# Performance work log

Hardware: AMD Instinct MI355X
Metric: run time of the kernel (lower is better)

The kernel has to match this reference:

```python
import jax, jax.numpy as jnp
import numpy as np

N = 4096
DIM_IN = 256
DIM_H = DIM_IN // 2  # 128
DIM_OUT = 128


def setup_inputs() -> dict:
    key = jax.random.key(0)
    ks = jax.random.split(key, 8)
    # Normalized-adjacency-like dense matrices (scaled so propagation is stable
    # and exp() of the score matrix does not overflow).
    A_s = jax.random.uniform(ks[0], (N, N), dtype=jnp.float32) * (1.0 / N)
    A_t = jax.random.uniform(ks[1], (N, N), dtype=jnp.float32) * (1.0 / N)
    X_s = jax.random.normal(ks[2], (N, DIM_IN), dtype=jnp.float32) * 0.1
    X_t = jax.random.normal(ks[3], (N, DIM_IN), dtype=jnp.float32) * 0.1
    # Linear weights (bias=False). Stored as [in, out] for x @ W.
    W1 = jax.random.normal(ks[4], (DIM_IN, DIM_H), dtype=jnp.float32) / np.sqrt(DIM_IN)
    W2 = jax.random.normal(ks[5], (DIM_H, DIM_H), dtype=jnp.float32) / np.sqrt(DIM_H)
    W3 = jax.random.normal(ks[6], (DIM_H, DIM_H), dtype=jnp.float32) / np.sqrt(DIM_H)
    W4 = jax.random.normal(ks[7], (DIM_H, DIM_OUT), dtype=jnp.float32) / np.sqrt(DIM_H)
    return {"A_s": A_s, "X_s": X_s, "A_t": A_t, "X_t": X_t,
            "W1": W1, "W2": W2, "W3": W3, "W4": W4}


def reference(A_s, X_s, A_t, X_t, W1, W2, W3, W4):
    # Two GCN propagation layers per graph: relu((A @ X) @ W)
    Xs = jax.nn.relu((A_s @ X_s) @ W1)   # [N, DIM_H]
    Xs = jax.nn.relu((A_s @ Xs) @ W2)    # [N, DIM_H]
    Xt = jax.nn.relu((A_t @ X_t) @ W1)
    Xt = jax.nn.relu((A_t @ Xt) @ W2)
    # Unnormalized exp cross-attention scores: [N, N]
    S = jnp.exp((Xs @ W3) @ Xt.T)
    out_s = (S @ Xs) @ W4                # [N, DIM_OUT]
    out_t = (S @ Xt) @ W4                # [N, DIM_OUT]
    return (out_s, out_t, S)
```

## Files before the change

kernel.cpp:

```cpp
#include <hip/hip_runtime.h>
#include <stdint.h>

typedef __attribute__((ext_vector_type(4))) float f32x4;
typedef __attribute__((ext_vector_type(8))) short s16x8;

typedef const __attribute__((address_space(1))) void* gas_ptr;
typedef __attribute__((address_space(3))) void* las_ptr;

__device__ __forceinline__ unsigned short f2b(float f) {
    union { float f; unsigned u; } v; v.f = f;
    unsigned r = v.u + 0x7fffu + ((v.u >> 16) & 1u);
    return (unsigned short)(r >> 16);
}

__device__ __forceinline__ unsigned pack2(float f0, float f1) {
    union { float f; unsigned u; } a, b;
    a.f = f0; b.f = f1;
    return __builtin_amdgcn_perm(b.u + 0x8000u, a.u + 0x8000u, 0x07060302u);
}

__global__ void cast2_bf16_k(const float* __restrict__ a, unsigned short* __restrict__ da,
                             const float* __restrict__ b, unsigned short* __restrict__ db,
                             int n4) {
    int i = blockIdx.x * blockDim.x + threadIdx.x;
    int stride = gridDim.x * blockDim.x;
    for (; i < n4; i += stride) {
        float4 va = ((const float4*)a)[i];
        ushort4 pa; pa.x = f2b(va.x); pa.y = f2b(va.y); pa.z = f2b(va.z); pa.w = f2b(va.w);
        ((ushort4*)da)[i] = pa;
        float4 vb = ((const float4*)b)[i];
        ushort4 pb; pb.x = f2b(vb.x); pb.y = f2b(vb.y); pb.z = f2b(vb.z); pb.w = f2b(vb.w);
        ((ushort4*)db)[i] = pb;
    }
}

__global__ void reduce8_relu_cast_k(const float* __restrict__ P, unsigned short* __restrict__ d,
                                    int n4, int slice4) {
    int i = blockIdx.x * blockDim.x + threadIdx.x;
    int stride = gridDim.x * blockDim.x;
    for (; i < n4; i += stride) {
        f32x4 s = ((const f32x4*)P)[i];
        #pragma unroll
        for (int z = 1; z < 8; z++) s += ((const f32x4*)P)[i + (size_t)z * slice4];
        ushort4 p;
        p.x = f2b(fmaxf(s[0], 0.f)); p.y = f2b(fmaxf(s[1], 0.f));
        p.z = f2b(fmaxf(s[2], 0.f)); p.w = f2b(fmaxf(s[3], 0.f));
        ((ushort4*)d)[i] = p;
    }
}

__global__ void reduce8_fold_k(const float* __restrict__ P, float* __restrict__ out) {
    const int n4 = 4096 * 256 / 4;
    int i = blockIdx.x * blockDim.x + threadIdx.x;
    int stride = gridDim.x * blockDim.x;
    for (; i < n4; i += stride) {
        f32x4 s = ((const f32x4*)P)[i];
        #pragma unroll
        for (int z = 1; z < 8; z++) s += ((const f32x4*)P)[i + (size_t)z * n4];
        const int m = i >> 6;
        const int c = (i & 63) << 2;
        float* o = out + ((c >> 7) ? (size_t)4096 * 128 : 0) + (size_t)m * 128 + (c & 127);
        *(f32x4*)(void*)o = s;
    }
}

__global__ void transpose_w_k(const float* __restrict__ W1, const float* __restrict__ W2,
                              const float* __restrict__ W3, const float* __restrict__ W4,
                              unsigned short* __restrict__ W1t, unsigned short* __restrict__ W2t,
                              unsigned short* __restrict__ W3t, unsigned short* __restrict__ W4t) {
    __shared__ float tile[32][33];
    const float* src; unsigned short* dst; int R, C;
    switch (blockIdx.z) {
        case 0: src = W1; dst = W1t; R = 256; C = 128; break;
        case 1: src = W2; dst = W2t; R = 128; C = 128; break;
        case 2: src = W3; dst = W3t; R = 128; C = 128; break;
        default: src = W4; dst = W4t; R = 128; C = 128; break;
    }
    int c0 = blockIdx.x * 32, r0 = blockIdx.y * 32;
    if (r0 >= R) return;
    int tx = threadIdx.x & 31, ty = threadIdx.x >> 5;
    #pragma unroll
    for (int rr = ty; rr < 32; rr += 8)
        tile[rr][tx] = src[(size_t)(r0 + rr) * C + c0 + tx];
    __syncthreads();
    #pragma unroll
    for (int rr = ty; rr < 32; rr += 8)
        dst[(size_t)(c0 + rr) * R + r0 + tx] = f2b(tile[tx][rr]);
}

enum { EP_BF16 = 0, EP_T = 1, EP_TFOLD = 2, EP_EXP = 3, EP_PART = 4 };

template<int BM, int BN, int FM, int FN, int EPI>
__global__ void __launch_bounds__(256)
gemm_nt(const unsigned short* __restrict__ A, const unsigned short* __restrict__ B,
        int lda, int ldb, int kchunk,
        float* __restrict__ Cf, unsigned short* __restrict__ Cb,
        unsigned short* __restrict__ Ct, int ldc, int ldct)
{
    __shared__ __align__(16) short As[BM * 32];
    __shared__ __align__(16) short Bs[BN * 32];

    const int t = threadIdx.x;
    const int lane = t & 63;
    const int w = t >> 6;
    const int wr = w >> 1, wc = w & 1;
    const int m0 = blockIdx.x * BM;
    const int n0 = blockIdx.y * BN;
    const int k0 = blockIdx.z * kchunk;

    f32x4 acc[FM][FN];
    #pragma unroll
    for (int i = 0; i < FM; i++)
        #pragma unroll
        for (int j = 0; j < FN; j++) acc[i][j] = (f32x4){0.f, 0.f, 0.f, 0.f};

    const int KT = kchunk >> 5;
    const int mrow = lane & 15;
    const int q8 = (lane >> 4) << 3;

    for (int kt = 0; kt < KT; ++kt) {
        const int kk = k0 + (kt << 5);
        #pragma unroll
        for (int idx = t; idx < BM * 4; idx += 256) {
            const unsigned short* g = A + (size_t)(m0 + (idx >> 2)) * lda + kk + ((idx & 3) << 3);
            __builtin_amdgcn_global_load_lds((gas_ptr)g, (las_ptr)(As + idx * 8), 16, 0, 0);
        }
        #pragma unroll
        for (int idx = t; idx < BN * 4; idx += 256) {
            const unsigned short* g = B + (size_t)(n0 + (idx >> 2)) * ldb + kk + ((idx & 3) << 3);
            __builtin_amdgcn_global_load_lds((gas_ptr)g, (las_ptr)(Bs + idx * 8), 16, 0, 0);
        }
        __syncthreads();

        s16x8 af[FM], bfr[FN];
        #pragma unroll
        for (int i = 0; i < FM; i++)
            af[i] = *(const s16x8*)(const void*)(As + (wr * FM * 16 + i * 16 + mrow) * 32 + q8);
        #pragma unroll
        for (int j = 0; j < FN; j++)
            bfr[j] = *(const s16x8*)(const void*)(Bs + (wc * FN * 16 + j * 16 + mrow) * 32 + q8);
        #pragma unroll
        for (int i = 0; i < FM; i++)
            #pragma unroll
            for (int j = 0; j < FN; j++)
                acc[i][j] = __builtin_amdgcn_mfma_f32_16x16x32_bf16(af[i], bfr[j], acc[i][j], 0, 0, 0);
        __syncthreads();
    }

    const int cn = lane & 15;
    const int q4 = (lane >> 4) << 2;
    #pragma unroll
    for (int i = 0; i < FM; i++) {
        const int mb = m0 + wr * FM * 16 + i * 16 + q4;
        #pragma unroll
        for (int j = 0; j < FN; j++) {
            const int nn = n0 + wc * FN * 16 + j * 16 + cn;
            if constexpr (EPI == EP_BF16) {
                #pragma unroll
                for (int r = 0; r < 4; r++)
                    Cb[(size_t)(mb + r) * ldc + nn] = f2b(acc[i][j][r]);
            } else if constexpr (EPI == EP_T) {
                ushort4 p;
                p.x = f2b(acc[i][j][0]); p.y = f2b(acc[i][j][1]);
                p.z = f2b(acc[i][j][2]); p.w = f2b(acc[i][j][3]);
                *(ushort4*)(void*)(Ct + (size_t)nn * ldct + mb) = p;
            } else if constexpr (EPI == EP_TFOLD) {
                ushort4 p;
                p.x = f2b(acc[i][j][0]); p.y = f2b(acc[i][j][1]);
                p.z = f2b(acc[i][j][2]); p.w = f2b(acc[i][j][3]);
                const int trow = nn + ((mb >> 12) << 7);
                *(ushort4*)(void*)(Ct + (size_t)trow * ldct + (mb & 4095)) = p;
            } else if constexpr (EPI == EP_EXP) {
                #pragma unroll
                for (int r = 0; r < 4; r++) {
                    float v = __expf(acc[i][j][r]);
                    Cf[(size_t)(mb + r) * ldc + nn] = v;
                    Cb[(size_t)(mb + r) * ldc + nn] = f2b(v);
                }
            } else if constexpr (EPI == EP_PART) {
                float* base = Cf + (size_t)blockIdx.z * ((size_t)4096 * 256);
                #pragma unroll
                for (int r = 0; r < 4; r++)
                    base[(size_t)(mb + r) * ldc + nn] = acc[i][j][r];
            }
        }
    }
}

__global__ void __launch_bounds__(256)
pz_fused(const unsigned short* __restrict__ X2,
         const unsigned short* __restrict__ W3t, const unsigned short* __restrict__ W4t,
         unsigned short* __restrict__ Pb, unsigned short* __restrict__ ZcatT)
{
    const bool isP = (blockIdx.y == 1);
    if (isP && blockIdx.x >= 128) return;
    const unsigned short* B = isP ? W3t : W4t;

    __shared__ __align__(16) short As[32 * 32];
    __shared__ __align__(16) short Bs[128 * 32];

    const int t = threadIdx.x;
    const int lane = t & 63;
    const int w = t >> 6;
    const int wr = w >> 1, wc = w & 1;
    const int m0 = blockIdx.x * 32;

    f32x4 acc[4];
    #pragma unroll
    for (int j = 0; j < 4; j++) acc[j] = (f32x4){0.f, 0.f, 0.f, 0.f};

    const int mrow = lane & 15;
    const int q8 = (lane >> 4) << 3;

    for (int kt = 0; kt < 4; ++kt) {
        const int kk = kt << 5;
        if (t < 128) {
            const unsigned short* g = X2 + (size_t)(m0 + (t >> 2)) * 128 + kk + ((t & 3) << 3);
            __builtin_amdgcn_global_load_lds((gas_ptr)g, (las_ptr)(As + t * 8), 16, 0, 0);
        }
        #pragma unroll
        for (int idx = t; idx < 512; idx += 256) {
            const unsigned short* g = B + (size_t)(idx >> 2) * 128 + kk + ((idx & 3) << 3);
            __builtin_amdgcn_global_load_lds((gas_ptr)g, (las_ptr)(Bs + idx * 8), 16, 0, 0);
        }
        __syncthreads();

        s16x8 af = *(const s16x8*)(const void*)(As + (wr * 16 + mrow) * 32 + q8);
        #pragma unroll
        for (int j = 0; j < 4; j++) {
            s16x8 bf = *(const s16x8*)(const void*)(Bs + (wc * 64 + j * 16 + mrow) * 32 + q8);
            acc[j] = __builtin_amdgcn_mfma_f32_16x16x32_bf16(af, bf, acc[j], 0, 0, 0);
        }
        __syncthreads();
    }

    const int cn = lane & 15;
    const int q4 = (lane >> 4) << 2;
    const int mb = m0 + wr * 16 + q4;
    #pragma unroll
    for (int j = 0; j < 4; j++) {
        const int nn = wc * 64 + j * 16 + cn;
        if (isP) {
            #pragma unroll
            for (int r = 0; r < 4; r++)
                Pb[(size_t)(mb + r) * 128 + nn] = f2b(acc[j][r]);
        } else {
            ushort4 p;
            p.x = f2b(acc[j][0]); p.y = f2b(acc[j][1]);
            p.z = f2b(acc[j][2]); p.w = f2b(acc[j][3]);
            const int trow = nn + ((mb >> 12) << 7);
            *(ushort4*)(void*)(ZcatT + (size_t)trow * 4096 + (mb & 4095)) = p;
        }
    }
}

__global__ void __launch_bounds__(256)
gemm_a32_nt(const float* __restrict__ A, const float* __restrict__ A2,
            const unsigned short* __restrict__ B, const unsigned short* __restrict__ B2,
            int Mhalf, int lda, int ldb, int kchunk, float* __restrict__ Cf, int ldc)
{
    __shared__ __align__(16) float As[64 * 32];
    __shared__ __align__(16) short Bs[128 * 32];

    const int t = threadIdx.x;
    const int lane = t & 63;
    const int w = t >> 6;
    const int wr = w >> 1, wc = w & 1;
    const int m0 = blockIdx.x * 64;
    const int n0 = blockIdx.y * 128;
    const int k0 = blockIdx.z * kchunk;

    const float* Ap = A;
    const unsigned short* Bp = B;
    int am0 = m0;
    if (m0 >= Mhalf) { Ap = A2; Bp = B2; am0 = m0 - Mhalf; }

    f32x4 acc[2][4];
    #pragma unroll
    for (int i = 0; i < 2; i++)
        #pragma unroll
        for (int j = 0; j < 4; j++) acc[i][j] = (f32x4){0.f, 0.f, 0.f, 0.f};

    const int KT = kchunk >> 5;
    const int mrow = lane & 15;
    const int q8 = (lane >> 4) << 3;
    const int q2 = (lane >> 4) << 1;

    for (int kt = 0; kt < KT; ++kt) {
        const int kk = k0 + (kt << 5);
        #pragma unroll
        for (int it = 0; it < 2; ++it) {
            int idx = it * 256 + t;
            int row = idx >> 3, grp = idx & 7;
            const float* g = Ap + (size_t)(am0 + row) * lda + kk + ((grp ^ (row & 7)) << 2);
            __builtin_amdgcn_global_load_lds((gas_ptr)g, (las_ptr)(As + idx * 4), 16, 0, 0);
        }
        #pragma unroll
        for (int it = 0; it < 2; ++it) {
            int idx = it * 256 + t;
            const unsigned short* g = Bp + (size_t)(n0 + (idx >> 2)) * ldb + kk + ((idx & 3) << 3);
            __builtin_amdgcn_global_load_lds((gas_ptr)g, (las_ptr)(Bs + idx * 8), 16, 0, 0);
        }
        __syncthreads();

        s16x8 af[2], bfr[4];
        #pragma unroll
        for (int i = 0; i < 2; i++) {
            const int r = wr * 32 + i * 16 + mrow;
            const f32x4 lo = *(const f32x4*)(const void*)(As + r * 32 + ((q2 ^ (r & 7)) << 2));
            const f32x4 hi = *(const f32x4*)(const void*)(As + r * 32 + (((q2 | 1) ^ (r & 7)) << 2));
            union { s16x8 v; unsigned u[4]; } pk;
            pk.u[0] = pack2(lo[0], lo[1]); pk.u[1] = pack2(lo[2], lo[3]);
            pk.u[2] = pack2(hi[0], hi[1]); pk.u[3] = pack2(hi[2], hi[3]);
            af[i] = pk.v;
        }
        #pragma unroll
        for (int j = 0; j < 4; j++)
            bfr[j] = *(const s16x8*)(const void*)(Bs + (wc * 64 + j * 16 + mrow) * 32 + q8);
        #pragma unroll
        for (int i = 0; i < 2; i++)
            #pragma unroll
            for (int j = 0; j < 4; j++)
                acc[i][j] = __builtin_amdgcn_mfma_f32_16x16x32_bf16(af[i], bfr[j], acc[i][j], 0, 0, 0);
        __syncthreads();
    }

    float* base = Cf + (size_t)blockIdx.z * ((size_t)8192 * 128);
    const int cn = lane & 15;
    const int q4 = (lane >> 4) << 2;
    #pragma unroll
    for (int i = 0; i < 2; i++) {
        const int mb = m0 + wr * 32 + i * 16 + q4;
        #pragma unroll
        for (int j = 0; j < 4; j++) {
            const int nn = n0 + wc * 64 + j * 16 + cn;
            #pragma unroll
            for (int r = 0; r < 4; r++)
                base[(size_t)(mb + r) * ldc + nn] = acc[i][j][r];
        }
    }
}

extern "C" void kernel_launch(void* const* d_in, const int* in_sizes, int n_in,
                              void* d_out, int out_size, void* d_ws, size_t ws_size,
                              hipStream_t stream) {
    const int N = 4096;
    const float* A_s = (const float*)d_in[0];
    const float* X_s = (const float*)d_in[1];
    const float* A_t = (const float*)d_in[2];
    const float* X_t = (const float*)d_in[3];
    const float* W1  = (const float*)d_in[4];
    const float* W2  = (const float*)d_in[5];
    const float* W3  = (const float*)d_in[6];
    const float* W4  = (const float*)d_in[7];

    float* out   = (float*)d_out;
    float* S_out = out + (size_t)2 * N * 128;

    char* ws = (char*)d_ws;
    unsigned short* Xcatb = (unsigned short*)(ws + 0);
    unsigned short* W1t   = (unsigned short*)(ws + 4194304);
    unsigned short* W2t   = (unsigned short*)(ws + 4259840);
    unsigned short* W3t   = (unsigned short*)(ws + 4292608);
    unsigned short* W4t   = (unsigned short*)(ws + 4325376);
    unsigned short* Y1T   = (unsigned short*)(ws + 4718592);
    unsigned short* X1b   = (unsigned short*)(ws + 6815744);
    unsigned short* X2b   = (unsigned short*)(ws + 8912896);
    unsigned short* Pb    = (unsigned short*)(ws + 11010048);
    unsigned short* ZcatT = (unsigned short*)(ws + 12058624);
    float*          Pf    = (float*)(ws + 14155776);
    unsigned short* Sb    = (unsigned short*)(ws + 47710208);
    unsigned short* Xt2b  = X2b + (size_t)N * 128;

    cast2_bf16_k<<<512, 256, 0, stream>>>(X_s, Xcatb, X_t, Xcatb + (size_t)N * 256, N * 256 / 4);
    transpose_w_k<<<dim3(4, 8, 4), 256, 0, stream>>>(W1, W2, W3, W4, W1t, W2t, W3t, W4t);

    gemm_nt<32, 128, 1, 4, EP_T><<<dim3(256, 1, 1), 256, 0, stream>>>(
        Xcatb, W1t, 256, 256, 256, nullptr, nullptr, Y1T, 0, 8192);

    gemm_a32_nt<<<dim3(128, 1, 8), 256, 0, stream>>>(
        A_s, A_t, Y1T, Y1T + 4096, 4096, 4096, 8192, 512, Pf, 128);
    reduce8_relu_cast_k<<<1024, 256, 0, stream>>>(Pf, X1b, 8192 * 128 / 4, 8192 * 128 / 4);

    gemm_nt<32, 128, 1, 4, EP_T><<<dim3(256, 1, 1), 256, 0, stream>>>(
        X1b, W2t, 128, 128, 128, nullptr, nullptr, Y1T, 0, 8192);

    gemm_a32_nt<<<dim3(128, 1, 8), 256, 0, stream>>>(
        A_s, A_t, Y1T, Y1T + 4096, 4096, 4096, 8192, 512, Pf, 128);
    reduce8_relu_cast_k<<<1024, 256, 0, stream>>>(Pf, X2b, 8192 * 128 / 4, 8192 * 128 / 4);

    pz_fused<<<dim3(256, 2, 1), 256, 0, stream>>>(X2b, W3t, W4t, Pb, ZcatT);

    gemm_nt<128, 128, 4, 4, EP_EXP><<<dim3(32, 32, 1), 256, 0, stream>>>(
        Pb, Xt2b, 128, 128, 128, S_out, Sb, nullptr, 4096, 0);

    gemm_nt<64, 128, 2, 4, EP_PART><<<dim3(64, 2, 8), 256, 0, stream>>>(
        Sb, ZcatT, 4096, 4096, 512, Pf, nullptr, nullptr, 256, 0);
    reduce8_fold_k<<<1024, 256, 0, stream>>>(Pf, out);
}
```

Before: 312.2 us.

## Unify GEMMs into register-loaded A with wide swizzled LDS B stages

Replaces the separate bf16 and fp32-A GEMM kernels with one templated kernel. A fragments are read straight from global memory into registers, with fp32-to-bf16 packing done in registers for the adjacency matrices. B is staged into LDS in wide K slabs (128–256) using an XOR swizzle, so there are far fewer barriers per K step. The aim is to cut LDS traffic and synchronisation overhead. The cost is uncoalesced per-lane global reads of A, which may lean on the cache, plus higher register and LDS use per block.

```diff
diff --git a/kernel.cpp b/kernel.cpp
--- a/kernel.cpp
+++ b/kernel.cpp
@@ -88,63 +88,90 @@
         dst[(size_t)(c0 + rr) * R + r0 + tx] = f2b(tile[tx][rr]);
 }
 
-enum { EP_BF16 = 0, EP_T = 1, EP_TFOLD = 2, EP_EXP = 3, EP_PART = 4 };
-
-template<int BM, int BN, int FM, int FN, int EPI>
+enum { EP_T = 1, EP_EXP = 3, EP_PART = 4 };
+
+template<int BM, int FM, int KS, int NSTAGE, bool AF32, int EPI, bool DUAL>
 __global__ void __launch_bounds__(256)
-gemm_nt(const unsigned short* __restrict__ A, const unsigned short* __restrict__ B,
-        int lda, int ldb, int kchunk,
-        float* __restrict__ Cf, unsigned short* __restrict__ Cb,
-        unsigned short* __restrict__ Ct, int ldc, int ldct)
+gemm_areg(const void* __restrict__ Av, const void* __restrict__ A2v,
+          const unsigned short* __restrict__ B, const unsigned short* __restrict__ B2,
+          int Mhalf, int lda, int ldb,
+          float* __restrict__ Cf, unsigned short* __restrict__ Cb,
+          unsigned short* __restrict__ Ct, int ldc, int ldct, size_t zstride)
 {
-    __shared__ __align__(16) short As[BM * 32];
-    __shared__ __align__(16) short Bs[BN * 32];
+    constexpr int SEG = KS / 8;
+    __shared__ __align__(16) short Bs[128 * KS];
 
     const int t = threadIdx.x;
     const int lane = t & 63;
     const int w = t >> 6;
     const int wr = w >> 1, wc = w & 1;
     const int m0 = blockIdx.x * BM;
-    const int n0 = blockIdx.y * BN;
-    const int k0 = blockIdx.z * kchunk;
-
-    f32x4 acc[FM][FN];
+    const int n0 = blockIdx.y * 128;
+    const int k0 = blockIdx.z * (KS * NSTAGE);
+
+    const float* Af = (const float*)Av;
+    const unsigned short* Ab = (const unsigned short*)Av;
+    const unsigned short* Bp = B;
+    int am0 = m0;
+    if constexpr (DUAL) {
+        if (m0 >= Mhalf) {
+            Af = (const float*)A2v; Ab = (const unsigned short*)A2v;
+            Bp = B2; am0 = m0 - Mhalf;
+        }
+    }
+
+    f32x4 acc[FM][4];
     #pragma unroll
     for (int i = 0; i < FM; i++)
         #pragma unroll
-        for (int j = 0; j < FN; j++) acc[i][j] = (f32x4){0.f, 0.f, 0.f, 0.f};
-
-    const int KT = kchunk >> 5;
+        for (int j = 0; j < 4; j++) acc[i][j] = (f32x4){0.f, 0.f, 0.f, 0.f};
+
     const int mrow = lane & 15;
-    const int q8 = (lane >> 4) << 3;
-
-    for (int kt = 0; kt < KT; ++kt) {
-        const int kk = k0 + (kt << 5);
-        #pragma unroll
-        for (int idx = t; idx < BM * 4; idx += 256) {
-            const unsigned short* g = A + (size_t)(m0 + (idx >> 2)) * lda + kk + ((idx & 3) << 3);
-            __builtin_amdgcn_global_load_lds((gas_ptr)g, (las_ptr)(As + idx * 8), 16, 0, 0);
-        }
-        #pragma unroll
-        for (int idx = t; idx < BN * 4; idx += 256) {
-            const unsigned short* g = B + (size_t)(n0 + (idx >> 2)) * ldb + kk + ((idx & 3) << 3);
+    const int q = lane >> 4;
+
+    for (int st = 0; st < NSTAGE; ++st) {
+        const int kk = k0 + st * KS;
+        if (st) __syncthreads();
+        #pragma unroll
+        for (int it = 0; it < SEG / 2; ++it) {
+            const int idx = it * 256 + t;
+            const int row = idx / SEG, seg = idx % SEG;
+            const int gseg = seg ^ (row & 7);
+            const unsigned short* g = Bp + (size_t)(n0 + row) * ldb + kk + (gseg << 3);
             __builtin_amdgcn_global_load_lds((gas_ptr)g, (las_ptr)(Bs + idx * 8), 16, 0, 0);
         }
         __syncthreads();
 
-        s16x8 af[FM], bfr[FN];
-        #pragma unroll
-        for (int i = 0; i < FM; i++)
-            af[i] = *(const s16x8*)(const void*)(As + (wr * FM * 16 + i * 16 + mrow) * 32 + q8);
-        #pragma unroll
-        for (int j = 0; j < FN; j++)
-            bfr[j] = *(const s16x8*)(const void*)(Bs + (wc * FN * 16 + j * 16 + mrow) * 32 + q8);
-        #pragma unroll
-        for (int i = 0; i < FM; i++)
+        #pragma unroll
+        for (int ks = 0; ks < KS / 32; ++ks) {
+            const int kbase = kk + ks * 32 + q * 8;
+            s16x8 af[FM], bfr[4];
             #pragma unroll
-            for (int j = 0; j < FN; j++)
-                acc[i][j] = __builtin_amdgcn_mfma_f32_16x16x32_bf16(af[i], bfr[j], acc[i][j], 0, 0, 0);
-        __syncthreads();
+            for (int i = 0; i < FM; i++) {
+                const int r = am0 + wr * FM * 16 + i * 16 + mrow;
+                if constexpr (AF32) {
+                    const f32x4 lo = *(const f32x4*)(const void*)(Af + (size_t)r * lda + kbase);
+                    const f32x4 hi = *(const f32x4*)(const void*)(Af + (size_t)r * lda + kbase + 4);
+                    union { s16x8 v; unsigned u[4]; } pk;
+                    pk.u[0] = pack2(lo[0], lo[1]); pk.u[1] = pack2(lo[2], lo[3]);
+                    pk.u[2] = pack2(hi[0], hi[1]); pk.u[3] = pack2(hi[2], hi[3]);
+                    af[i] = pk.v;
+                } else {
+                    af[i] = *(const s16x8*)(const void*)(Ab + (size_t)r * lda + kbase);
+                }
+            }
+            #pragma unroll
+            for (int j = 0; j < 4; j++) {
+                const int rb = wc * 64 + j * 16 + mrow;
+                const int sg = (ks * 4 + q) ^ (rb & 7);
+                bfr[j] = *(const s16x8*)(const void*)(Bs + rb * KS + (sg << 3));
+            }
+            #pragma unroll
+            for (int i = 0; i < FM; i++)
+                #pragma unroll
+                for (int j = 0; j < 4; j++)
+                    acc[i][j] = __builtin_amdgcn_mfma_f32_16x16x32_bf16(af[i], bfr[j], acc[i][j], 0, 0, 0);
+        }
     }
 
     const int cn = lane & 15;
@@ -153,23 +180,13 @@
     for (int i = 0; i < FM; i++) {
         const int mb = m0 + wr * FM * 16 + i * 16 + q4;
         #pragma unroll
-        for (int j = 0; j < FN; j++) {
-            const int nn = n0 + wc * FN * 16 + j * 16 + cn;
-            if constexpr (EPI == EP_BF16) {
-                #pragma unroll
-                for (int r = 0; r < 4; r++)
-                    Cb[(size_t)(mb + r) * ldc + nn] = f2b(acc[i][j][r]);
-            } else if constexpr (EPI == EP_T) {
+        for (int j = 0; j < 4; j++) {
+            const int nn = n0 + wc * 64 + j * 16 + cn;
+            if constexpr (EPI == EP_T) {
                 ushort4 p;
                 p.x = f2b(acc[i][j][0]); p.y = f2b(acc[i][j][1]);
                 p.z = f2b(acc[i][j][2]); p.w = f2b(acc[i][j][3]);
                 *(ushort4*)(void*)(Ct + (size_t)nn * ldct + mb) = p;
-            } else if constexpr (EPI == EP_TFOLD) {
-                ushort4 p;
-                p.x = f2b(acc[i][j][0]); p.y = f2b(acc[i][j][1]);
-                p.z = f2b(acc[i][j][2]); p.w = f2b(acc[i][j][3]);
-                const int trow = nn + ((mb >> 12) << 7);
-                *(ushort4*)(void*)(Ct + (size_t)trow * ldct + (mb & 4095)) = p;
             } else if constexpr (EPI == EP_EXP) {
                 #pragma unroll
                 for (int r = 0; r < 4; r++) {
@@ -178,7 +195,7 @@
                     Cb[(size_t)(mb + r) * ldc + nn] = f2b(v);
                 }
             } else if constexpr (EPI == EP_PART) {
-                float* base = Cf + (size_t)blockIdx.z * ((size_t)4096 * 256);
+                float* base = Cf + (size_t)blockIdx.z * zstride;
                 #pragma unroll
                 for (int r = 0; r < 4; r++)
                     base[(size_t)(mb + r) * ldc + nn] = acc[i][j][r];
@@ -214,6 +231,7 @@
 
     for (int kt = 0; kt < 4; ++kt) {
         const int kk = kt << 5;
+        if (kt) __syncthreads();
         if (t < 128) {
             const unsigned short* g = X2 + (size_t)(m0 + (t >> 2)) * 128 + kk + ((t & 3) << 3);
             __builtin_amdgcn_global_load_lds((gas_ptr)g, (las_ptr)(As + t * 8), 16, 0, 0);
@@ -231,7 +249,6 @@
             s16x8 bf = *(const s16x8*)(const void*)(Bs + (wc * 64 + j * 16 + mrow) * 32 + q8);
             acc[j] = __builtin_amdgcn_mfma_f32_16x16x32_bf16(af, bf, acc[j], 0, 0, 0);
         }
-        __syncthreads();
     }
 
     const int cn = lane & 15;
@@ -250,93 +267,6 @@
             p.z = f2b(acc[j][2]); p.w = f2b(acc[j][3]);
             const int trow = nn + ((mb >> 12) << 7);
             *(ushort4*)(void*)(ZcatT + (size_t)trow * 4096 + (mb & 4095)) = p;
-        }
-    }
-}
-
-__global__ void __launch_bounds__(256)
-gemm_a32_nt(const float* __restrict__ A, const float* __restrict__ A2,
-            const unsigned short* __restrict__ B, const unsigned short* __restrict__ B2,
-            int Mhalf, int lda, int ldb, int kchunk, float* __restrict__ Cf, int ldc)
-{
-    __shared__ __align__(16) float As[64 * 32];
-    __shared__ __align__(16) short Bs[128 * 32];
-
-    const int t = threadIdx.x;
-    const int lane = t & 63;
-    const int w = t >> 6;
-    const int wr = w >> 1, wc = w & 1;
-    const int m0 = blockIdx.x * 64;
-    const int n0 = blockIdx.y * 128;
-    const int k0 = blockIdx.z * kchunk;
-
-    const float* Ap = A;
-    const unsigned short* Bp = B;
-    int am0 = m0;
-    if (m0 >= Mhalf) { Ap = A2; Bp = B2; am0 = m0 - Mhalf; }
-
-    f32x4 acc[2][4];
-    #pragma unroll
-    for (int i = 0; i < 2; i++)
-        #pragma unroll
-        for (int j = 0; j < 4; j++) acc[i][j] = (f32x4){0.f, 0.f, 0.f, 0.f};
-
-    const int KT = kchunk >> 5;
-    const int mrow = lane & 15;
-    const int q8 = (lane >> 4) << 3;
-    const int q2 = (lane >> 4) << 1;
-
-    for (int kt = 0; kt < KT; ++kt) {
-        const int kk = k0 + (kt << 5);
-        #pragma unroll
-        for (int it = 0; it < 2; ++it) {
-            int idx = it * 256 + t;
-            int row = idx >> 3, grp = idx & 7;
-            const float* g = Ap + (size_t)(am0 + row) * lda + kk + ((grp ^ (row & 7)) << 2);
-            __builtin_amdgcn_global_load_lds((gas_ptr)g, (las_ptr)(As + idx * 4), 16, 0, 0);
-        }
-        #pragma unroll
-        for (int it = 0; it < 2; ++it) {
-            int idx = it * 256 + t;
-            const unsigned short* g = Bp + (size_t)(n0 + (idx >> 2)) * ldb + kk + ((idx & 3) << 3);
-            __builtin_amdgcn_global_load_lds((gas_ptr)g, (las_ptr)(Bs + idx * 8), 16, 0, 0);
-        }
-        __syncthreads();
-
-        s16x8 af[2], bfr[4];
-        #pragma unroll
-        for (int i = 0; i < 2; i++) {
-            const int r = wr * 32 + i * 16 + mrow;
-            const f32x4 lo = *(const f32x4*)(const void*)(As + r * 32 + ((q2 ^ (r & 7)) << 2));
-            const f32x4 hi = *(const f32x4*)(const void*)(As + r * 32 + (((q2 | 1) ^ (r & 7)) << 2));
-            union { s16x8 v; unsigned u[4]; } pk;
-            pk.u[0] = pack2(lo[0], lo[1]); pk.u[1] = pack2(lo[2], lo[3]);
-            pk.u[2] = pack2(hi[0], hi[1]); pk.u[3] = pack2(hi[2], hi[3]);
-            af[i] = pk.v;
-        }
-        #pragma unroll
-        for (int j = 0; j < 4; j++)
-            bfr[j] = *(const s16x8*)(const void*)(Bs + (wc * 64 + j * 16 + mrow) * 32 + q8);
-        #pragma unroll
-        for (int i = 0; i < 2; i++)
-            #pragma unroll
-            for (int j = 0; j < 4; j++)
-                acc[i][j] = __builtin_amdgcn_mfma_f32_16x16x32_bf16(af[i], bfr[j], acc[i][j], 0, 0, 0);
-        __syncthreads();
-    }
-
-    float* base = Cf + (size_t)blockIdx.z * ((size_t)8192 * 128);
-    const int cn = lane & 15;
-    const int q4 = (lane >> 4) << 2;
-    #pragma unroll
-    for (int i = 0; i < 2; i++) {
-        const int mb = m0 + wr * 32 + i * 16 + q4;
-        #pragma unroll
-        for (int j = 0; j < 4; j++) {
-            const int nn = n0 + wc * 64 + j * 16 + cn;
-            #pragma unroll
-            for (int r = 0; r < 4; r++)
-                base[(size_t)(mb + r) * ldc + nn] = acc[i][j][r];
         }
     }
 }
@@ -375,26 +305,32 @@
     cast2_bf16_k<<<512, 256, 0, stream>>>(X_s, Xcatb, X_t, Xcatb + (size_t)N * 256, N * 256 / 4);
     transpose_w_k<<<dim3(4, 8, 4), 256, 0, stream>>>(W1, W2, W3, W4, W1t, W2t, W3t, W4t);
 
-    gemm_nt<32, 128, 1, 4, EP_T><<<dim3(256, 1, 1), 256, 0, stream>>>(
-        Xcatb, W1t, 256, 256, 256, nullptr, nullptr, Y1T, 0, 8192);
-
-    gemm_a32_nt<<<dim3(128, 1, 8), 256, 0, stream>>>(
-        A_s, A_t, Y1T, Y1T + 4096, 4096, 4096, 8192, 512, Pf, 128);
+    gemm_areg<32, 1, 256, 1, false, EP_T, false><<<dim3(256, 1, 1), 256, 0, stream>>>(
+        Xcatb, nullptr, W1t, nullptr, 0, 256, 256,
+        nullptr, nullptr, Y1T, 0, 8192, 0);
+
+    gemm_areg<64, 2, 256, 2, true, EP_PART, true><<<dim3(128, 1, 8), 256, 0, stream>>>(
+        A_s, A_t, Y1T, Y1T + 4096, 4096, 4096, 8192,
+        Pf, nullptr, nullptr, 128, 0, (size_t)8192 * 128);
     reduce8_relu_cast_k<<<1024, 256, 0, stream>>>(Pf, X1b, 8192 * 128 / 4, 8192 * 128 / 4);
 
-    gemm_nt<32, 128, 1, 4, EP_T><<<dim3(256, 1, 1), 256, 0, stream>>>(
-        X1b, W2t, 128, 128, 128, nullptr, nullptr, Y1T, 0, 8192);
-
-    gemm_a32_nt<<<dim3(128, 1, 8), 256, 0, stream>>>(
-        A_s, A_t, Y1T, Y1T + 4096, 4096, 4096, 8192, 512, Pf, 128);
+    gemm_areg<32, 1, 128, 1, false, EP_T, false><<<dim3(256, 1, 1), 256, 0, stream>>>(
+        X1b, nullptr, W2t, nullptr, 0, 128, 128,
+        nullptr, nullptr, Y1T, 0, 8192, 0);
+
+    gemm_areg<64, 2, 256, 2, true, EP_PART, true><<<dim3(128, 1, 8), 256, 0, stream>>>(
+        A_s, A_t, Y1T, Y1T + 4096, 4096, 4096, 8192,
+        Pf, nullptr, nullptr, 128, 0, (size_t)8192 * 128);
     reduce8_relu_cast_k<<<1024, 256, 0, stream>>>(Pf, X2b, 8192 * 128 / 4, 8192 * 128 / 4);
 
     pz_fused<<<dim3(256, 2, 1), 256, 0, stream>>>(X2b, W3t, W4t, Pb, ZcatT);
 
-    gemm_nt<128, 128, 4, 4, EP_EXP><<<dim3(32, 32, 1), 256, 0, stream>>>(
-        Pb, Xt2b, 128, 128, 128, S_out, Sb, nullptr, 4096, 0);
-
-    gemm_nt<64, 128, 2, 4, EP_PART><<<dim3(64, 2, 8), 256, 0, stream>>>(
-        Sb, ZcatT, 4096, 4096, 512, Pf, nullptr, nullptr, 256, 0);
+    gemm_areg<128, 4, 128, 1, false, EP_EXP, false><<<dim3(32, 32, 1), 256, 0, stream>>>(
+        Pb, nullptr, Xt2b, nullptr, 0, 128, 128,
+        S_out, Sb, nullptr, 4096, 0, 0);
+
+    gemm_areg<64, 2, 256, 2, false, EP_PART, false><<<dim3(64, 2, 8), 256, 0, stream>>>(
+        Sb, nullptr, ZcatT, nullptr, 0, 4096, 4096,
+        Pf, nullptr, nullptr, 256, 0, (size_t)4096 * 256);
     reduce8_fold_k<<<1024, 256, 0, stream>>>(Pf, out);
 }
```

After: 344.8 us. 10.4% more time.

## Cache bf16 copy of adjacency in first propagation, reuse it in second

Applied to the files above, without the earlier changes.

The first propagation GEMM now also writes the bf16-packed A_s/A_t tiles into a workspace buffer. The second propagation reads that bf16 copy instead of the fp32 matrices, which halves its A-side traffic. LDS loads for B and bf16 A get an XOR swizzle, S is stored with nontemporal stores, and the S@Z GEMM moves to 128-row tiles. The extra bf16 write (64 MB) adds traffic to the first GEMM, the new path depends on workspace size, and it reuses the Sb region.

```diff
diff --git a/kernel.cpp b/kernel.cpp
--- a/kernel.cpp
+++ b/kernel.cpp
@@ -174,7 +174,7 @@
                 #pragma unroll
                 for (int r = 0; r < 4; r++) {
                     float v = __expf(acc[i][j][r]);
-                    Cf[(size_t)(mb + r) * ldc + nn] = v;
+                    __builtin_nontemporal_store(v, Cf + (size_t)(mb + r) * ldc + nn);
                     Cb[(size_t)(mb + r) * ldc + nn] = f2b(v);
                 }
             } else if constexpr (EPI == EP_PART) {
@@ -254,12 +254,15 @@
     }
 }
 
+template<bool AF32, bool EMIT>
 __global__ void __launch_bounds__(256)
-gemm_a32_nt(const float* __restrict__ A, const float* __restrict__ A2,
-            const unsigned short* __restrict__ B, const unsigned short* __restrict__ B2,
-            int Mhalf, int lda, int ldb, int kchunk, float* __restrict__ Cf, int ldc)
+gemm_prop(const void* __restrict__ Av, const void* __restrict__ A2v,
+          const unsigned short* __restrict__ B, const unsigned short* __restrict__ B2,
+          int Mhalf, int lda, int ldb, int kchunk,
+          float* __restrict__ Cf, unsigned short* __restrict__ Aout)
 {
-    __shared__ __align__(16) float As[64 * 32];
+    __shared__ __align__(16) float Asf[AF32 ? 64 * 32 : 1];
+    __shared__ __align__(16) short Asb[AF32 ? 1 : 64 * 32];
     __shared__ __align__(16) short Bs[128 * 32];
 
     const int t = threadIdx.x;
@@ -267,13 +270,16 @@
     const int w = t >> 6;
     const int wr = w >> 1, wc = w & 1;
     const int m0 = blockIdx.x * 64;
-    const int n0 = blockIdx.y * 128;
     const int k0 = blockIdx.z * kchunk;
 
-    const float* Ap = A;
+    const float* Af = (const float*)Av;
+    const unsigned short* Ab = (const unsigned short*)Av;
     const unsigned short* Bp = B;
     int am0 = m0;
-    if (m0 >= Mhalf) { Ap = A2; Bp = B2; am0 = m0 - Mhalf; }
+    if (m0 >= Mhalf) {
+        Af = (const float*)A2v; Ab = (const unsigned short*)A2v;
+        Bp = B2; am0 = AF32 ? (m0 - Mhalf) : m0;
+    }
 
     f32x4 acc[2][4];
     #pragma unroll
@@ -283,22 +289,35 @@
 
     const int KT = kchunk >> 5;
     const int mrow = lane & 15;
-    const int q8 = (lane >> 4) << 3;
-    const int q2 = (lane >> 4) << 1;
+    const int q = lane >> 4;
+    const int q8 = q << 3;
+    const int q2 = q << 1;
 
     for (int kt = 0; kt < KT; ++kt) {
         const int kk = k0 + (kt << 5);
+        if constexpr (AF32) {
+            #pragma unroll
+            for (int it = 0; it < 2; ++it) {
+                int idx = it * 256 + t;
+                int row = idx >> 3, seg = idx & 7;
+                int gseg = seg ^ (row & 7);
+                const float* g = Af + (size_t)(am0 + row) * lda + kk + (gseg << 2);
+                __builtin_amdgcn_global_load_lds((gas_ptr)g, (las_ptr)(Asf + idx * 4), 16, 0, 0);
+            }
+        } else {
+            {
+                int row = t >> 2, seg = t & 3;
+                int gseg = seg ^ (row & 3);
+                const unsigned short* g = Ab + (size_t)(am0 + row) * lda + kk + (gseg << 3);
+                __builtin_amdgcn_global_load_lds((gas_ptr)g, (las_ptr)(Asb + t * 8), 16, 0, 0);
+            }
+        }
         #pragma unroll
         for (int it = 0; it < 2; ++it) {
             int idx = it * 256 + t;
-            int row = idx >> 3, grp = idx & 7;
-            const float* g = Ap + (size_t)(am0 + row) * lda + kk + ((grp ^ (row & 7)) << 2);
-            __builtin_amdgcn_global_load_lds((gas_ptr)g, (las_ptr)(As + idx * 4), 16, 0, 0);
-        }
-        #pragma unroll
-        for (int it = 0; it < 2; ++it) {
-            int idx = it * 256 + t;
-            const unsigned short* g = Bp + (size_t)(n0 + (idx >> 2)) * ldb + kk + ((idx & 3) << 3);
+            int row = idx >> 2, seg = idx & 3;
+            int gseg = seg ^ (row & 3);
+            const unsigned short* g = Bp + (size_t)(row) * ldb + kk + (gseg << 3);
             __builtin_amdgcn_global_load_lds((gas_ptr)g, (las_ptr)(Bs + idx * 8), 16, 0, 0);
         }
         __syncthreads();
@@ -307,16 +326,26 @@
         #pragma unroll
         for (int i = 0; i < 2; i++) {
             const int r = wr * 32 + i * 16 + mrow;
-            const f32x4 lo = *(const f32x4*)(const void*)(As + r * 32 + ((q2 ^ (r & 7)) << 2));
-            const f32x4 hi = *(const f32x4*)(const void*)(As + r * 32 + (((q2 | 1) ^ (r & 7)) << 2));
-            union { s16x8 v; unsigned u[4]; } pk;
-            pk.u[0] = pack2(lo[0], lo[1]); pk.u[1] = pack2(lo[2], lo[3]);
-            pk.u[2] = pack2(hi[0], hi[1]); pk.u[3] = pack2(hi[2], hi[3]);
-            af[i] = pk.v;
-        }
-        #pragma unroll
-        for (int j = 0; j < 4; j++)
-            bfr[j] = *(const s16x8*)(const void*)(Bs + (wc * 64 + j * 16 + mrow) * 32 + q8);
+            if constexpr (AF32) {
+                const f32x4 lo = *(const f32x4*)(const void*)(Asf + r * 32 + ((q2 ^ (r & 7)) << 2));
+                const f32x4 hi = *(const f32x4*)(const void*)(Asf + r * 32 + (((q2 | 1) ^ (r & 7)) << 2));
+                union { s16x8 v; unsigned u[4]; } pk;
+                pk.u[0] = pack2(lo[0], lo[1]); pk.u[1] = pack2(lo[2], lo[3]);
+                pk.u[2] = pack2(hi[0], hi[1]); pk.u[3] = pack2(hi[2], hi[3]);
+                af[i] = pk.v;
+                if constexpr (EMIT) {
+                    if (wc == 0)
+                        *(s16x8*)(void*)(Aout + (size_t)(m0 + r) * 4096 + kk + q8) = af[i];
+                }
+            } else {
+                af[i] = *(const s16x8*)(const void*)(Asb + r * 32 + ((q ^ (r & 3)) << 3));
+            }
+        }
+        #pragma unroll
+        for (int j = 0; j < 4; j++) {
+            const int rb = wc * 64 + j * 16 + mrow;
+            bfr[j] = *(const s16x8*)(const void*)(Bs + rb * 32 + ((q ^ (rb & 3)) << 3));
+        }
         #pragma unroll
         for (int i = 0; i < 2; i++)
             #pragma unroll
@@ -333,10 +362,10 @@
         const int mb = m0 + wr * 32 + i * 16 + q4;
         #pragma unroll
         for (int j = 0; j < 4; j++) {
-            const int nn = n0 + wc * 64 + j * 16 + cn;
+            const int nn = wc * 64 + j * 16 + cn;
             #pragma unroll
             for (int r = 0; r < 4; r++)
-                base[(size_t)(mb + r) * ldc + nn] = acc[i][j][r];
+                base[(size_t)(mb + r) * 128 + nn] = acc[i][j][r];
         }
     }
 }
@@ -370,7 +399,10 @@
     unsigned short* ZcatT = (unsigned short*)(ws + 12058624);
     float*          Pf    = (float*)(ws + 14155776);
     unsigned short* Sb    = (unsigned short*)(ws + 47710208);
+    unsigned short* Acatb = (unsigned short*)(ws + 47710208);
     unsigned short* Xt2b  = X2b + (size_t)N * 128;
+
+    const bool big = ws_size >= (size_t)47710208 + (size_t)8192 * 4096 * 2;
 
     cast2_bf16_k<<<512, 256, 0, stream>>>(X_s, Xcatb, X_t, Xcatb + (size_t)N * 256, N * 256 / 4);
     transpose_w_k<<<dim3(4, 8, 4), 256, 0, stream>>>(W1, W2, W3, W4, W1t, W2t, W3t, W4t);
@@ -378,15 +410,23 @@
     gemm_nt<32, 128, 1, 4, EP_T><<<dim3(256, 1, 1), 256, 0, stream>>>(
         Xcatb, W1t, 256, 256, 256, nullptr, nullptr, Y1T, 0, 8192);
 
-    gemm_a32_nt<<<dim3(128, 1, 8), 256, 0, stream>>>(
-        A_s, A_t, Y1T, Y1T + 4096, 4096, 4096, 8192, 512, Pf, 128);
+    if (big)
+        gemm_prop<true, true><<<dim3(128, 1, 8), 256, 0, stream>>>(
+            A_s, A_t, Y1T, Y1T + 4096, 4096, 4096, 8192, 512, Pf, Acatb);
+    else
+        gemm_prop<true, false><<<dim3(128, 1, 8), 256, 0, stream>>>(
+            A_s, A_t, Y1T, Y1T + 4096, 4096, 4096, 8192, 512, Pf, nullptr);
     reduce8_relu_cast_k<<<1024, 256, 0, stream>>>(Pf, X1b, 8192 * 128 / 4, 8192 * 128 / 4);
 
     gemm_nt<32, 128, 1, 4, EP_T><<<dim3(256, 1, 1), 256, 0, stream>>>(
         X1b, W2t, 128, 128, 128, nullptr, nullptr, Y1T, 0, 8192);
 
-    gemm_a32_nt<<<dim3(128, 1, 8), 256, 0, stream>>>(
-        A_s, A_t, Y1T, Y1T + 4096, 4096, 4096, 8192, 512, Pf, 128);
+    if (big)
+        gemm_prop<false, false><<<dim3(128, 1, 8), 256, 0, stream>>>(
+            Acatb, Acatb, Y1T, Y1T + 4096, 4096, 4096, 8192, 512, Pf, nullptr);
+    else
+        gemm_prop<true, false><<<dim3(128, 1, 8), 256, 0, stream>>>(
+            A_s, A_t, Y1T, Y1T + 4096, 4096, 4096, 8192, 512, Pf, nullptr);
     reduce8_relu_cast_k<<<1024, 256, 0, stream>>>(Pf, X2b, 8192 * 128 / 4, 8192 * 128 / 4);
 
     pz_fused<<<dim3(256, 2, 1), 256, 0, stream>>>(X2b, W3t, W4t, Pb, ZcatT);
@@ -394,7 +434,7 @@
     gemm_nt<128, 128, 4, 4, EP_EXP><<<dim3(32, 32, 1), 256, 0, stream>>>(
         Pb, Xt2b, 128, 128, 128, S_out, Sb, nullptr, 4096, 0);
 
-    gemm_nt<64, 128, 2, 4, EP_PART><<<dim3(64, 2, 8), 256, 0, stream>>>(
+    gemm_nt<128, 128, 4, 4, EP_PART><<<dim3(32, 2, 8), 256, 0, stream>>>(
         Sb, ZcatT, 4096, 4096, 512, Pf, nullptr, nullptr, 256, 0);
     reduce8_fold_k<<<1024, 256, 0, stream>>>(Pf, out);
 }
```

Measured after the change: 313.4 us. No clear change (+0.4%).
